# Optimization experiments

Measured on AMD Instinct MI355X. Metric: run time of the kernel, lower is better.

## Reference

```python
import jax, jax.numpy as jnp
import numpy as np

B, S, H, HD = 8, 1024, 16, 64
D = H * HD
NINF = -10000.0
EPS = 1e-6


def setup_inputs() -> dict:
    key = jax.random.key(0)
    ks = jax.random.split(key, 6)
    std = 0.02
    return {
        "x": jax.random.normal(ks[0], (B, S, D), jnp.float32),
        "mask": jax.random.randint(ks[1], (B, S), 0, 2, jnp.int32),
        "wq": jax.random.normal(ks[2], (D, D), jnp.float32) * std,
        "bq": jnp.zeros((D,), jnp.float32),
        "wk": jax.random.normal(ks[3], (D, D), jnp.float32) * std,
        "bk": jnp.zeros((D,), jnp.float32),
        "wv": jax.random.normal(ks[4], (D, D), jnp.float32) * std,
        "bv": jnp.zeros((D,), jnp.float32),
        "wo": jax.random.normal(ks[5], (D, D), jnp.float32) * std,
        "bo": jnp.zeros((D,), jnp.float32),
        "gamma": jnp.ones((D,), jnp.float32),
        "beta": jnp.zeros((D,), jnp.float32),
    }


def _heads(t):
    # [B,S,D] -> [B,H,S,HD]
    return t.reshape(t.shape[0], t.shape[1], H, HD).transpose(0, 2, 1, 3)


def _layernorm(x, gamma, beta):
    mu = jnp.mean(x, -1, keepdims=True)
    var = jnp.mean(jnp.square(x - mu), -1, keepdims=True)
    return (x - mu) * jax.lax.rsqrt(var + EPS) * gamma + beta


def reference(x, mask, wq, bq, wk, bk, wv, bv, wo, bo, gamma, beta):
    q = _heads(x @ wq + bq)
    k = _heads(x @ wk + bk)
    v = _heads(x @ wv + bv)
    scores = jnp.einsum("bhqd,bhkd->bhqk", q, k) / np.sqrt(HD).astype(np.float32)
    # padding mask broadcast over key axis: 1 = masked
    scores = scores + mask.astype(jnp.float32)[:, None, None, :] * NINF
    attn = jax.nn.softmax(scores, axis=-1)
    ctx = jnp.einsum("bhqk,bhkd->bhqd", attn, v)  # [B,H,S,HD]
    ctx = ctx.transpose(0, 2, 1, 3).reshape(B, S, D)
    out = _layernorm(x + ctx @ wo + bo, gamma, beta)
    return out
```

## Files before the change

### kernel.cpp

```cpp
#include <hip/hip_runtime.h>
#include <stdint.h>

typedef unsigned short u16;
typedef unsigned int u32;
typedef __bf16 b16x8 __attribute__((ext_vector_type(8)));
typedef float f32x4 __attribute__((ext_vector_type(4)));

#define B_ 8
#define S_ 1024
#define H_ 16
#define HD_ 64
#define D_ 1024
#define M_ 8192

__device__ __forceinline__ u16 f2bf(float f) {
  u32 u = __float_as_uint(f);
  return (u16)((u + 0x7fffu + ((u >> 16) & 1u)) >> 16);
}

__device__ __forceinline__ f32x4 mfma16(b16x8 a, b16x8 b, f32x4 c) {
  return __builtin_amdgcn_mfma_f32_16x16x32_bf16(a, b, c, 0, 0, 0);
}

__device__ __forceinline__ void cp16(const u16* g, u16* l) {
  __builtin_amdgcn_global_load_lds(
      (const __attribute__((address_space(1))) u32*)(g),
      (__attribute__((address_space(3))) u32*)(l), 16, 0, 0);
}

__global__ __launch_bounds__(1024) void wconv_kernel(
    const float* __restrict__ w0, const float* __restrict__ w1,
    const float* __restrict__ w2, const float* __restrict__ w3,
    u16* __restrict__ t0, u16* __restrict__ t1, u16* __restrict__ t2,
    u16* __restrict__ t3) {
  __shared__ float tile[32][33];
  const int z = blockIdx.z;
  const float* src = (z == 0) ? w0 : (z == 1) ? w1 : (z == 2) ? w2 : w3;
  u16* dst = (z == 0) ? t0 : (z == 1) ? t1 : (z == 2) ? t2 : t3;
  const int tx = threadIdx.x, ty = threadIdx.y;
  const int x0 = blockIdx.x * 32, y0 = blockIdx.y * 32;
  tile[ty][tx] = src[(size_t)(y0 + ty) * D_ + x0 + tx];
  __syncthreads();
  dst[(size_t)(x0 + ty) * D_ + y0 + tx] = f2bf(tile[tx][ty]);
}

__global__ __launch_bounds__(256) void xconv_kernel(const float* __restrict__ x,
                                                    u16* __restrict__ xb) {
  const size_t i = ((size_t)blockIdx.x * 256 + threadIdx.x) * 4;
  const float4 v = *(const float4*)(x + i);
  u16 o[4] = {f2bf(v.x), f2bf(v.y), f2bf(v.z), f2bf(v.w)};
  uint2 pack;
  pack.x = ((u32)o[1] << 16) | o[0];
  pack.y = ((u32)o[3] << 16) | o[2];
  *(uint2*)(xb + i) = pack;
}

__device__ __forceinline__ void gemm128_mainloop(
    const u16* __restrict__ A, const u16* __restrict__ BT, int K, int m0,
    int n0, u16* lds, f32x4 (&acc)[4][4]) {
  const int t = threadIdx.x;
  const int lane = t & 63;
  const int w = t >> 6;
  const int l15 = lane & 15;
  const int q4 = lane >> 4;
  const int mwave = (w >> 1) * 64;
  const int nwave = (w & 1) * 64;

  u16* Alds = lds;
  u16* Blds = lds + 8192;

  const f32x4 zero = {0.f, 0.f, 0.f, 0.f};
  for (int mt = 0; mt < 4; ++mt)
    for (int nt = 0; nt < 4; ++nt) acc[mt][nt] = zero;

  const int rbase = t >> 3;
  const int scol = ((t & 7) ^ (rbase & 7)) * 8;
  const u16* Ag = A + (size_t)(m0 + rbase) * K + scol;
  const u16* Bg = BT + (size_t)(n0 + rbase) * K + scol;

  const int sx = l15 & 7;
  const int cA0 = ((0 * 4 + q4) ^ sx) * 8;
  const int cA1 = ((1 * 4 + q4) ^ sx) * 8;

  for (int k0 = 0; k0 < K; k0 += 64) {
    __syncthreads();
    for (int c = 0; c < 4; ++c) {
      cp16(Ag + (size_t)(c * 32) * K + k0, Alds + c * 2048 + t * 8);
      cp16(Bg + (size_t)(c * 32) * K + k0, Blds + c * 2048 + t * 8);
    }
    __syncthreads();

    b16x8 af[4][2], bfr[4][2];
    for (int mt = 0; mt < 4; ++mt) {
      const int row = (mwave + mt * 16 + l15) * 64;
      af[mt][0] = *(const b16x8*)(Alds + row + cA0);
      af[mt][1] = *(const b16x8*)(Alds + row + cA1);
    }
    for (int nt = 0; nt < 4; ++nt) {
      const int row = (nwave + nt * 16 + l15) * 64;
      bfr[nt][0] = *(const b16x8*)(Blds + row + cA0);
      bfr[nt][1] = *(const b16x8*)(Blds + row + cA1);
    }
    for (int mt = 0; mt < 4; ++mt)
      for (int nt = 0; nt < 4; ++nt) {
        acc[mt][nt] = mfma16(af[mt][0], bfr[nt][0], acc[mt][nt]);
        acc[mt][nt] = mfma16(af[mt][1], bfr[nt][1], acc[mt][nt]);
      }
  }
}

__global__ __launch_bounds__(256) void qkv_gemm_kernel(
    const u16* __restrict__ xb, const u16* __restrict__ wtq,
    const u16* __restrict__ wtk, const u16* __restrict__ wtv,
    const float* __restrict__ bq, const float* __restrict__ bk,
    const float* __restrict__ bv, u16* __restrict__ Q, u16* __restrict__ Kb,
    u16* __restrict__ VT) {
  __shared__ __align__(16) u16 lds[16384];
  const int z = blockIdx.z;
  const u16* BTp = (z == 0) ? wtq : (z == 1) ? wtk : wtv;
  const float* bias = (z == 0) ? bq : (z == 1) ? bk : bv;
  u16* out = (z == 0) ? Q : (z == 1) ? Kb : VT;
  const int m0 = blockIdx.y * 128, n0 = blockIdx.x * 128;

  f32x4 acc[4][4];
  gemm128_mainloop(xb, BTp, D_, m0, n0, lds, acc);

  const int lane = threadIdx.x & 63, w = threadIdx.x >> 6;
  const int l15 = lane & 15, q4 = lane >> 4;
  const int mwave = (w >> 1) * 64, nwave = (w & 1) * 64;

  for (int nt = 0; nt < 4; ++nt) {
    const int n = n0 + nwave + nt * 16 + l15;
    const float bias_v = bias[n];
    const int h = n >> 6, hd = n & 63;
    for (int mt = 0; mt < 4; ++mt) {
      for (int r = 0; r < 4; ++r) {
        const int m = m0 + mwave + mt * 16 + q4 * 4 + r;
        const int b = m >> 10, s = m & 1023;
        const float v = acc[mt][nt][r] + bias_v;
        size_t idx;
        if (z < 2)
          idx = (((size_t)(b * H_ + h)) * S_ + s) * HD_ + hd;
        else
          idx = (((size_t)(b * H_ + h)) * HD_ + hd) * S_ + s;
        out[idx] = f2bf(v);
      }
    }
  }
}

#define PAD_ 68
__global__ __launch_bounds__(256) void attn_kernel(
    const u16* __restrict__ Q, const u16* __restrict__ Kb,
    const u16* __restrict__ VT, const int* __restrict__ mask,
    u16* __restrict__ ctx) {
  __shared__ __align__(16) u16 QPlds[64 * PAD_];
  __shared__ __align__(16) u16 Klds[64 * PAD_];
  __shared__ __align__(16) u16 Vlds[64 * PAD_];

  const int t = threadIdx.x;
  const int lane = t & 63, w = t >> 6;
  const int l15 = lane & 15, q4 = lane >> 4;
  const int bh = blockIdx.y;
  const int b = bh >> 4, h = bh & 15;
  const int q0 = blockIdx.x * 64;

  const u16* Qbh = Q + (size_t)bh * S_ * HD_;
  const u16* Kbh = Kb + (size_t)bh * S_ * HD_;
  const u16* Vbh = VT + (size_t)bh * S_ * HD_;
  const int* maskb = mask + b * S_;

  const int srow = t >> 3, scol = (t & 7) * 8;
  {
    b16x8 q0v = *(const b16x8*)(Qbh + (size_t)(q0 + srow) * HD_ + scol);
    b16x8 q1v = *(const b16x8*)(Qbh + (size_t)(q0 + srow + 32) * HD_ + scol);
    *(b16x8*)(QPlds + srow * PAD_ + scol) = q0v;
    *(b16x8*)(QPlds + (srow + 32) * PAD_ + scol) = q1v;
  }
  __syncthreads();
  b16x8 aq[2];
  aq[0] = *(const b16x8*)(QPlds + (w * 16 + l15) * PAD_ + q4 * 8);
  aq[1] = *(const b16x8*)(QPlds + (w * 16 + l15) * PAD_ + 32 + q4 * 8);

  const f32x4 zero = {0.f, 0.f, 0.f, 0.f};
  f32x4 acc[4];
  for (int nt = 0; nt < 4; ++nt) acc[nt] = zero;
  float lsum[4] = {0.f, 0.f, 0.f, 0.f};
  u16* Pw = QPlds + w * 16 * PAD_;
  const float c1 = 0.18033688f;

  for (int j = 0; j < 16; ++j) {
    const int key0 = j * 64;
    b16x8 k0v = *(const b16x8*)(Kbh + (size_t)(key0 + srow) * HD_ + scol);
    b16x8 k1v = *(const b16x8*)(Kbh + (size_t)(key0 + srow + 32) * HD_ + scol);
    b16x8 v0v = *(const b16x8*)(Vbh + (size_t)srow * S_ + key0 + scol);
    b16x8 v1v = *(const b16x8*)(Vbh + (size_t)(srow + 32) * S_ + key0 + scol);
    float madd[4];
    for (int nt = 0; nt < 4; ++nt)
      madd[nt] = -14427.0f * (float)maskb[key0 + nt * 16 + l15];
    __syncthreads();
    *(b16x8*)(Klds + srow * PAD_ + scol) = k0v;
    *(b16x8*)(Klds + (srow + 32) * PAD_ + scol) = k1v;
    *(b16x8*)(Vlds + srow * PAD_ + scol) = v0v;
    *(b16x8*)(Vlds + (srow + 32) * PAD_ + scol) = v1v;
    __syncthreads();

    f32x4 sf[4];
    for (int nt = 0; nt < 4; ++nt) sf[nt] = zero;
    for (int kk = 0; kk < 2; ++kk)
      for (int nt = 0; nt < 4; ++nt) {
        b16x8 bk =
            *(const b16x8*)(Klds + (nt * 16 + l15) * PAD_ + kk * 32 + q4 * 8);
        sf[nt] = mfma16(aq[kk], bk, sf[nt]);
      }

    for (int nt = 0; nt < 4; ++nt)
      for (int r = 0; r < 4; ++r) {
        const float p = __builtin_amdgcn_exp2f(sf[nt][r] * c1 + madd[nt]);
        lsum[r] += p;
        Pw[(q4 * 4 + r) * PAD_ + nt * 16 + l15] = f2bf(p);
      }
    asm volatile("s_waitcnt lgkmcnt(0)" ::: "memory");

    for (int kk = 0; kk < 2; ++kk) {
      b16x8 ap = *(const b16x8*)(Pw + l15 * PAD_ + kk * 32 + q4 * 8);
      for (int nt = 0; nt < 4; ++nt) {
        b16x8 vb =
            *(const b16x8*)(Vlds + (nt * 16 + l15) * PAD_ + kk * 32 + q4 * 8);
        acc[nt] = mfma16(ap, vb, acc[nt]);
      }
    }
  }

  for (int r = 0; r < 4; ++r)
    for (int off = 1; off < 16; off <<= 1) lsum[r] += __shfl_xor(lsum[r], off);

  for (int nt = 0; nt < 4; ++nt) {
    const int dcol = h * 64 + nt * 16 + l15;
    for (int r = 0; r < 4; ++r) {
      const int srw = q0 + w * 16 + q4 * 4 + r;
      const float o = acc[nt][r] / lsum[r];
      ctx[((size_t)(b * S_ + srw)) * D_ + dcol] = f2bf(o);
    }
  }
}

__global__ __launch_bounds__(256) void out_gemm_kernel(
    const u16* __restrict__ ctx, const u16* __restrict__ wto,
    const float* __restrict__ bo, const float* __restrict__ x,
    float* __restrict__ y) {
  __shared__ __align__(16) u16 lds[16384];
  const int m0 = blockIdx.y * 128, n0 = blockIdx.x * 128;
  f32x4 acc[4][4];
  gemm128_mainloop(ctx, wto, D_, m0, n0, lds, acc);

  const int lane = threadIdx.x & 63, w = threadIdx.x >> 6;
  const int l15 = lane & 15, q4 = lane >> 4;
  const int mwave = (w >> 1) * 64, nwave = (w & 1) * 64;

  for (int nt = 0; nt < 4; ++nt) {
    const int n = n0 + nwave + nt * 16 + l15;
    const float bias = bo[n];
    for (int mt = 0; mt < 4; ++mt) {
      for (int r = 0; r < 4; ++r) {
        const int m = m0 + mwave + mt * 16 + q4 * 4 + r;
        y[(size_t)m * D_ + n] = acc[mt][nt][r] + bias + x[(size_t)m * D_ + n];
      }
    }
  }
}

__global__ __launch_bounds__(256) void ln_kernel(const float* __restrict__ y,
                                                 const float* __restrict__ g,
                                                 const float* __restrict__ be,
                                                 float* __restrict__ out) {
  const int row = blockIdx.x, t = threadIdx.x;
  const float* yr = y + (size_t)row * D_;
  const float4 v = *(const float4*)(yr + t * 4);
  float s = v.x + v.y + v.z + v.w;
  float ss = v.x * v.x + v.y * v.y + v.z * v.z + v.w * v.w;
  for (int off = 1; off < 64; off <<= 1) {
    s += __shfl_xor(s, off);
    ss += __shfl_xor(ss, off);
  }
  __shared__ float red[8];
  const int w = t >> 6, lane = t & 63;
  if (lane == 0) {
    red[w] = s;
    red[4 + w] = ss;
  }
  __syncthreads();
  s = red[0] + red[1] + red[2] + red[3];
  ss = red[4] + red[5] + red[6] + red[7];
  const float mu = s * (1.f / 1024.f);
  const float var = ss * (1.f / 1024.f) - mu * mu;
  const float rs = rsqrtf(var + 1e-6f);
  const int c = t * 4;
  const float4 gv = *(const float4*)(g + c);
  const float4 bv = *(const float4*)(be + c);
  float4 o;
  o.x = (v.x - mu) * rs * gv.x + bv.x;
  o.y = (v.y - mu) * rs * gv.y + bv.y;
  o.z = (v.z - mu) * rs * gv.z + bv.z;
  o.w = (v.w - mu) * rs * gv.w + bv.w;
  *(float4*)(out + (size_t)row * D_ + c) = o;
}

extern "C" void kernel_launch(void* const* d_in, const int* in_sizes, int n_in,
                              void* d_out, int out_size, void* d_ws,
                              size_t ws_size, hipStream_t stream) {
  const float* x = (const float*)d_in[0];
  const int* mask = (const int*)d_in[1];
  const float* wq = (const float*)d_in[2];
  const float* bq = (const float*)d_in[3];
  const float* wk = (const float*)d_in[4];
  const float* bk = (const float*)d_in[5];
  const float* wv = (const float*)d_in[6];
  const float* bv = (const float*)d_in[7];
  const float* wo = (const float*)d_in[8];
  const float* bo = (const float*)d_in[9];
  const float* gamma = (const float*)d_in[10];
  const float* beta = (const float*)d_in[11];
  float* out = (float*)d_out;

  char* ws = (char*)d_ws;
  const size_t MB = 1024ull * 1024ull;
  u16* wtq = (u16*)(ws + 0 * MB);
  u16* wtk = (u16*)(ws + 2 * MB);
  u16* wtv = (u16*)(ws + 4 * MB);
  u16* wto = (u16*)(ws + 6 * MB);
  u16* xb = (u16*)(ws + 8 * MB);
  u16* ctx = (u16*)(ws + 8 * MB);
  u16* Qb = (u16*)(ws + 24 * MB);
  u16* Kb = (u16*)(ws + 40 * MB);
  u16* VTb = (u16*)(ws + 56 * MB);
  float* y = (float*)(ws + 24 * MB);

  wconv_kernel<<<dim3(32, 32, 4), dim3(32, 32), 0, stream>>>(
      wq, wk, wv, wo, wtq, wtk, wtv, wto);
  xconv_kernel<<<8192, 256, 0, stream>>>(x, xb);
  qkv_gemm_kernel<<<dim3(8, 64, 3), 256, 0, stream>>>(
      xb, wtq, wtk, wtv, bq, bk, bv, Qb, Kb, VTb);
  attn_kernel<<<dim3(16, 128), 256, 0, stream>>>(Qb, Kb, VTb, mask, ctx);
  out_gemm_kernel<<<dim3(8, 64), 256, 0, stream>>>(ctx, wto, bo, x, y);
  ln_kernel<<<8192, 256, 0, stream>>>(y, gamma, beta, out);
}
```

Measured before the change: 334.7 us.

## Prefetch next K/V tile into registers and stage mask in LDS

The attention kernel now loads the next 64-key K/V tile from global memory into registers while the current tile is being computed, so global latency overlaps the MFMA and softmax work. The additive mask row is converted once into a shared-memory float array instead of being re-read from global memory on every iteration. It also uses the native bf16 conversion for P stores and multiplies by a reciprocal instead of dividing in the epilogue. This adds a 4 KB LDS buffer and extra live registers, which could lower occupancy.

```diff
diff --git a/kernel.cpp b/kernel.cpp
--- a/kernel.cpp
+++ b/kernel.cpp
@@ -157,6 +157,7 @@
   __shared__ __align__(16) u16 QPlds[64 * PAD_];
   __shared__ __align__(16) u16 Klds[64 * PAD_];
   __shared__ __align__(16) u16 Vlds[64 * PAD_];
+  __shared__ __align__(16) float Mlds[1024];
 
   const int t = threadIdx.x;
   const int lane = t & 63, w = t >> 6;
@@ -174,8 +175,15 @@
   {
     b16x8 q0v = *(const b16x8*)(Qbh + (size_t)(q0 + srow) * HD_ + scol);
     b16x8 q1v = *(const b16x8*)(Qbh + (size_t)(q0 + srow + 32) * HD_ + scol);
+    const int4 mv = *(const int4*)(maskb + t * 4);
     *(b16x8*)(QPlds + srow * PAD_ + scol) = q0v;
     *(b16x8*)(QPlds + (srow + 32) * PAD_ + scol) = q1v;
+    float4 mf;
+    mf.x = -14427.0f * (float)mv.x;
+    mf.y = -14427.0f * (float)mv.y;
+    mf.z = -14427.0f * (float)mv.z;
+    mf.w = -14427.0f * (float)mv.w;
+    *(float4*)(Mlds + t * 4) = mf;
   }
   __syncthreads();
   b16x8 aq[2];
@@ -189,21 +197,30 @@
   u16* Pw = QPlds + w * 16 * PAD_;
   const float c1 = 0.18033688f;
 
+  b16x8 kv0 = *(const b16x8*)(Kbh + (size_t)srow * HD_ + scol);
+  b16x8 kv1 = *(const b16x8*)(Kbh + (size_t)(srow + 32) * HD_ + scol);
+  b16x8 vv0 = *(const b16x8*)(Vbh + (size_t)srow * S_ + scol);
+  b16x8 vv1 = *(const b16x8*)(Vbh + (size_t)(srow + 32) * S_ + scol);
+
   for (int j = 0; j < 16; ++j) {
     const int key0 = j * 64;
-    b16x8 k0v = *(const b16x8*)(Kbh + (size_t)(key0 + srow) * HD_ + scol);
-    b16x8 k1v = *(const b16x8*)(Kbh + (size_t)(key0 + srow + 32) * HD_ + scol);
-    b16x8 v0v = *(const b16x8*)(Vbh + (size_t)srow * S_ + key0 + scol);
-    b16x8 v1v = *(const b16x8*)(Vbh + (size_t)(srow + 32) * S_ + key0 + scol);
+    __syncthreads();
+    *(b16x8*)(Klds + srow * PAD_ + scol) = kv0;
+    *(b16x8*)(Klds + (srow + 32) * PAD_ + scol) = kv1;
+    *(b16x8*)(Vlds + srow * PAD_ + scol) = vv0;
+    *(b16x8*)(Vlds + (srow + 32) * PAD_ + scol) = vv1;
+    __syncthreads();
+
+    if (j < 15) {
+      const int kn = key0 + 64;
+      kv0 = *(const b16x8*)(Kbh + (size_t)(kn + srow) * HD_ + scol);
+      kv1 = *(const b16x8*)(Kbh + (size_t)(kn + srow + 32) * HD_ + scol);
+      vv0 = *(const b16x8*)(Vbh + (size_t)srow * S_ + kn + scol);
+      vv1 = *(const b16x8*)(Vbh + (size_t)(srow + 32) * S_ + kn + scol);
+    }
+
     float madd[4];
-    for (int nt = 0; nt < 4; ++nt)
-      madd[nt] = -14427.0f * (float)maskb[key0 + nt * 16 + l15];
-    __syncthreads();
-    *(b16x8*)(Klds + srow * PAD_ + scol) = k0v;
-    *(b16x8*)(Klds + (srow + 32) * PAD_ + scol) = k1v;
-    *(b16x8*)(Vlds + srow * PAD_ + scol) = v0v;
-    *(b16x8*)(Vlds + (srow + 32) * PAD_ + scol) = v1v;
-    __syncthreads();
+    for (int nt = 0; nt < 4; ++nt) madd[nt] = Mlds[key0 + nt * 16 + l15];
 
     f32x4 sf[4];
     for (int nt = 0; nt < 4; ++nt) sf[nt] = zero;
@@ -218,7 +235,7 @@
       for (int r = 0; r < 4; ++r) {
         const float p = __builtin_amdgcn_exp2f(sf[nt][r] * c1 + madd[nt]);
         lsum[r] += p;
-        Pw[(q4 * 4 + r) * PAD_ + nt * 16 + l15] = f2bf(p);
+        *(__bf16*)(Pw + (q4 * 4 + r) * PAD_ + nt * 16 + l15) = (__bf16)p;
       }
     asm volatile("s_waitcnt lgkmcnt(0)" ::: "memory");
 
@@ -232,14 +249,16 @@
     }
   }
 
-  for (int r = 0; r < 4; ++r)
+  for (int r = 0; r < 4; ++r) {
     for (int off = 1; off < 16; off <<= 1) lsum[r] += __shfl_xor(lsum[r], off);
+    lsum[r] = 1.0f / lsum[r];
+  }
 
   for (int nt = 0; nt < 4; ++nt) {
     const int dcol = h * 64 + nt * 16 + l15;
     for (int r = 0; r < 4; ++r) {
       const int srw = q0 + w * 16 + q4 * 4 + r;
-      const float o = acc[nt][r] / lsum[r];
+      const float o = acc[nt][r] * lsum[r];
       ctx[((size_t)(b * S_ + srw)) * D_ + dcol] = f2bf(o);
     }
   }
```

Result: no change. 337.1 us (+0.7%).
